# Performance work log

Hardware: AMD Instinct MI355X
Metric: run time of the kernel (lower is better)

The kernel has to match this reference:

```python
import jax, jax.numpy as jnp
import numpy as np

IMG_SIZE = 224
PATCH_SIZE = 16
CONTEXT_LEN = 316
LATENT_DIM = 1024
NUM_HEADS = 16
NUM_PATCHES = (IMG_SIZE // PATCH_SIZE) ** 2  # 196
SEQ_LEN = NUM_PATCHES + CONTEXT_LEN          # 512
BATCH = 8


def prefix_lm_mask(num_img_patches, total):
    # lower-triangular causal mask, but the image-patch block is fully bidirectional
    m = np.tril(np.ones((total, total), dtype=np.float32))
    m[:num_img_patches, :num_img_patches] = 1.0
    return jnp.asarray(m)  # [S, S], 1 = attend, 0 = masked


def setup_inputs() -> dict:
    key = jax.random.key(0)
    k_x, k_q, k_k, k_v, k_o, k_b = jax.random.split(key, 6)
    d = LATENT_DIM
    scale = 1.0 / np.sqrt(d)
    return {
        "x": jax.random.normal(k_x, (BATCH, SEQ_LEN, d), dtype=jnp.float32),
        "w_q": jax.random.normal(k_q, (d, d), dtype=jnp.float32) * scale,
        "w_k": jax.random.normal(k_k, (d, d), dtype=jnp.float32) * scale,
        "w_v": jax.random.normal(k_v, (d, d), dtype=jnp.float32) * scale,
        "w_o": jax.random.normal(k_o, (d, d), dtype=jnp.float32) * scale,
        "b_o": jax.random.normal(k_b, (d,), dtype=jnp.float32) * 0.01,
    }


def reference(x, w_q, w_k, w_v, w_o, b_o):
    B, S, D = x.shape
    H = NUM_HEADS
    hd = D // H
    # projections (nn.Linear: y = x @ W^T)
    q = (x @ w_q.T).reshape(B, S, H, hd).transpose(0, 2, 1, 3)  # [B,H,S,hd]
    k = (x @ w_k.T).reshape(B, S, H, hd).transpose(0, 2, 1, 3)
    v = (x @ w_v.T).reshape(B, S, H, hd).transpose(0, 2, 1, 3)
    scores = jnp.einsum("bhqd,bhkd->bhqk", q, k) / jnp.sqrt(jnp.float32(hd))
    mask = prefix_lm_mask(NUM_PATCHES, S)  # [S,S]
    scores = jnp.where(mask == 0, jnp.float32(-jnp.inf), scores)
    attn = jax.nn.softmax(scores, axis=-1)
    ctx = jnp.einsum("bhqk,bhkd->bhqd", attn, v)
    ctx = ctx.transpose(0, 2, 1, 3).reshape(B, S, D)
    return ctx @ w_o.T + b_o
```

## Files before the change

### kernel.cpp

```cpp
#include <hip/hip_runtime.h>
#include <stdint.h>
#include <math.h>

#define NB_B 8
#define NB_S 512
#define NB_D 1024
#define NB_H 16
#define NB_HD 64
#define NP 196
#define MTOT 4096

#define OFF_XB 0
#define OFF_WQ 4194304
#define OFF_WK 5242880
#define OFF_WV 6291456
#define OFF_WO 7340032
#define OFF_Q  8388608
#define OFF_K  12582912
#define OFF_VT 16777216
#define OFF_CT 20971520

typedef __attribute__((ext_vector_type(8))) short bf16x8;
typedef __attribute__((ext_vector_type(4))) float f32x4;
typedef __attribute__((ext_vector_type(4))) short s16x4;

__device__ __forceinline__ short f2bf(float f) {
  union { float f; uint32_t u; } c; c.f = f;
  uint32_t r = (c.u + 0x7fffu + ((c.u >> 16) & 1u)) >> 16;
  return (short)r;
}

__device__ __forceinline__ uint32_t pack2bf(float lo, float hi) {
  uint32_t ulo = __float_as_uint(lo) + 0x8000u;
  uint32_t uhi = __float_as_uint(hi) + 0x8000u;
  return __builtin_amdgcn_perm(uhi, ulo, 0x07060302u);
}

__device__ __forceinline__ void async16(void* lds, const void* g) {
  __builtin_amdgcn_global_load_lds(
      (const __attribute__((address_space(1))) void*)g,
      (__attribute__((address_space(3))) void*)lds, 16, 0, 0);
}

__global__ __launch_bounds__(256) void cvt5(const float* __restrict__ x,
                                            const float* __restrict__ wq,
                                            const float* __restrict__ wk,
                                            const float* __restrict__ wv,
                                            const float* __restrict__ wo,
                                            short* __restrict__ ws) {
  int b = blockIdx.x, t = threadIdx.x;
  const float* src; short* dst; float scale;
  if (b < 4096) { src = x + b * 1024; dst = ws + OFF_XB + b * 1024; scale = 1.0f; }
  else {
    int wb = b - 4096, wi = wb >> 10, r = wb & 1023;
    switch (wi) {
      case 0:  src = wq + r * 1024; dst = ws + OFF_WQ + r * 1024; scale = 0.125f; break;
      case 1:  src = wk + r * 1024; dst = ws + OFF_WK + r * 1024; scale = 1.0f;   break;
      case 2:  src = wv + r * 1024; dst = ws + OFF_WV + r * 1024; scale = 1.0f;   break;
      default: src = wo + r * 1024; dst = ws + OFF_WO + r * 1024; scale = 1.0f;   break;
    }
  }
  int i = t << 2;
  float4 v = *(const float4*)(src + i);
  s16x4 o;
  o[0] = f2bf(v.x * scale); o[1] = f2bf(v.y * scale);
  o[2] = f2bf(v.z * scale); o[3] = f2bf(v.w * scale);
  *(s16x4*)(dst + i) = o;
}

__global__ __launch_bounds__(256, 2) void gemm_qkv(short* __restrict__ ws) {
  __shared__ __align__(16) short As[4096];
  __shared__ __align__(16) short Bs[4096];
  int bx = blockIdx.x;
  int wsel = bx >> 8;
  int tile = bx & 255;
  int mt = tile >> 3, nt = tile & 7;
  int m0 = mt << 7, n0 = nt << 7;
  const short* A  = ws + OFF_XB;
  const short* Bw = ws + (wsel == 0 ? OFF_WQ : (wsel == 1 ? OFF_WK : OFF_WV));
  int t = threadIdx.x, lane = t & 63, wvi = t >> 6;
  int c = lane & 15, quad = lane >> 4;
  int wm = wvi >> 1, wn = wvi & 1;
  f32x4 acc[4][4] = {};

  for (int kk = 0; kk < 1024; kk += 32) {
#pragma unroll
    for (int i = 0; i < 2; ++i) {
      int ch = wvi * 2 + i;
      const short* ga = A  + (m0 + ch * 16 + c) * 1024 + kk + (quad << 3);
      async16(&As[ch << 9], ga);
      const short* gb = Bw + (n0 + ch * 16 + c) * 1024 + kk + (quad << 3);
      async16(&Bs[ch << 9], gb);
    }
    __syncthreads();
    bf16x8 af[4], bfr[4];
#pragma unroll
    for (int i = 0; i < 4; ++i) af[i]  = *(const bf16x8*)&As[((wm * 4 + i) * 64 + lane) * 8];
#pragma unroll
    for (int j = 0; j < 4; ++j) bfr[j] = *(const bf16x8*)&Bs[((wn * 4 + j) * 64 + lane) * 8];
#pragma unroll
    for (int i = 0; i < 4; ++i)
#pragma unroll
      for (int j = 0; j < 4; ++j)
        acc[i][j] = __builtin_amdgcn_mfma_f32_16x16x32_bf16(af[i], bfr[j], acc[i][j], 0, 0, 0);
    __syncthreads();
  }

  short* outp = ws + (wsel == 0 ? OFF_Q : (wsel == 1 ? OFF_K : OFF_VT));
#pragma unroll
  for (int i = 0; i < 4; ++i) {
#pragma unroll
    for (int j = 0; j < 4; ++j) {
      int n = n0 + wn * 64 + j * 16 + c;
      int h = n >> 6, d = n & 63;
      int mq = m0 + wm * 64 + i * 16 + quad * 4;
      int bb = mq >> 9, s = mq & 511;
      if (wsel < 2) {
#pragma unroll
        for (int r = 0; r < 4; ++r)
          outp[((bb * 16 + h) * 512 + (s + r)) * 64 + d] = f2bf(acc[i][j][r]);
      } else {
        s16x4 o;
#pragma unroll
        for (int r = 0; r < 4; ++r) o[r] = f2bf(acc[i][j][r]);
        *(s16x4*)&outp[((bb * 16 + h) * 64 + d) * 512 + s] = o;
      }
    }
  }
}

__global__ __launch_bounds__(256, 2) void attn(short* __restrict__ ws) {
  __shared__ __align__(16) short Kb[4096];
  __shared__ __align__(16) short Vb[4096];
  int bi = blockIdx.x;
  int bh = bi >> 2, qcr = bi & 3;
  int qc = (qcr + bh + 2 * (bh >> 6)) & 3;
  int t = threadIdx.x, lane = t & 63, wvi = t >> 6;
  int c = lane & 15, quad = lane >> 4;
  const short* Qh  = ws + OFF_Q  + bh * (512 * 64);
  const short* Kh  = ws + OFF_K  + bh * (512 * 64);
  const short* Vth = ws + OFF_VT + bh * (64 * 512);
  short* ctx = ws + OFF_CT;
  int b = bh >> 4, h = bh & 15;

  int qt0 = qc * 128 + wvi * 32;
  int qt1 = qt0 + 16;
  int kn0 = (qt0 + 16 > NP) ? (qt0 + 16) : NP;
  int kn1 = (qt1 + 16 > NP) ? (qt1 + 16) : NP;
  int knb = (qc * 128 + 128 > NP) ? (qc * 128 + 128) : NP;
  int NCH = (knb + 63) >> 6;

  bf16x8 q00 = *(const bf16x8*)(Qh + (qt0 + c) * 64 + (quad << 3));
  bf16x8 q01 = *(const bf16x8*)(Qh + (qt0 + c) * 64 + 32 + (quad << 3));
  bf16x8 q10 = *(const bf16x8*)(Qh + (qt1 + c) * 64 + (quad << 3));
  bf16x8 q11 = *(const bf16x8*)(Qh + (qt1 + c) * 64 + 32 + (quad << 3));

  f32x4 acc0[4] = {}, acc1[4] = {};
  float l0 = 0.0f, l1 = 0.0f;
  int L0 = c + ((quad & 1) << 5);
  bool hilo = quad >= 2;

  for (int ch = 0; ch < NCH; ++ch) {
    int k0 = ch << 6;
    {
      const short* gk = Kh + (k0 + wvi * 16 + c) * 64 + (quad << 3);
      async16(&Kb[(wvi * 2 + 0) << 9], gk);
      async16(&Kb[(wvi * 2 + 1) << 9], gk + 32);
      const short* gv = Vth + (wvi * 16 + c) * 512 + k0 + (quad << 3);
      async16(&Vb[(wvi * 2 + 0) << 9], gv);
      async16(&Vb[(wvi * 2 + 1) << 9], gv + 32);
    }
    __syncthreads();

    bf16x8 ak[4][2], av[4][2];
#pragma unroll
    for (int mb = 0; mb < 4; ++mb)
#pragma unroll
      for (int f = 0; f < 2; ++f) {
        ak[mb][f] = *(const bf16x8*)&Kb[((mb * 2 + f) << 9) + lane * 8];
        av[mb][f] = *(const bf16x8*)&Vb[((mb * 2 + f) << 9) + lane * 8];
      }

#pragma unroll
    for (int s = 0; s < 2; ++s) {
      int qt = s ? qt1 : qt0;
      int kn = s ? kn1 : kn0;
      if (k0 >= kn) continue;
      bf16x8 bq0 = s ? q10 : q00;
      bf16x8 bq1 = s ? q11 : q01;
      f32x4* acc = s ? acc1 : acc0;

      float p[4][4];
#pragma unroll
      for (int mb = 0; mb < 4; ++mb) {
        f32x4 st = {};
        st = __builtin_amdgcn_mfma_f32_16x16x32_bf16(ak[mb][0], bq0, st, 0, 0, 0);
        st = __builtin_amdgcn_mfma_f32_16x16x32_bf16(ak[mb][1], bq1, st, 0, 0, 0);
#pragma unroll
        for (int r = 0; r < 4; ++r) p[mb][r] = __expf(st[r]);
      }

      if ((k0 + 64 > NP) && (k0 + 64 > qt + 1)) {
        int row = qt + c;
#pragma unroll
        for (int mb = 0; mb < 4; ++mb)
#pragma unroll
          for (int r = 0; r < 4; ++r) {
            int key = k0 + mb * 16 + (quad << 2) + r;
            bool v = (row < NP) ? (key < NP) : (key <= row);
            p[mb][r] = v ? p[mb][r] : 0.0f;
          }
      }
      float ls = 0.0f;
#pragma unroll
      for (int mb = 0; mb < 4; ++mb)
#pragma unroll
        for (int r = 0; r < 4; ++r) ls += p[mb][r];
      if (s) l1 += ls; else l0 += ls;

#pragma unroll
      for (int hh = 0; hh < 2; ++hh) {
        float* pa = p[2 * hh];
        float* pb = p[2 * hh + 1];
        uint32_t e0 = pack2bf(pa[0], pa[1]);
        uint32_t e1 = pack2bf(pa[2], pa[3]);
        uint32_t e2 = pack2bf(pb[0], pb[1]);
        uint32_t e3 = pack2bf(pb[2], pb[3]);
        uint32_t a0 = (uint32_t)__shfl((int)e0, L0);
        uint32_t b0 = (uint32_t)__shfl((int)e1, L0);
        uint32_t a1 = (uint32_t)__shfl((int)e0, L0 + 16);
        uint32_t b1 = (uint32_t)__shfl((int)e1, L0 + 16);
        uint32_t c0 = (uint32_t)__shfl((int)e2, L0);
        uint32_t d0 = (uint32_t)__shfl((int)e3, L0);
        uint32_t c1 = (uint32_t)__shfl((int)e2, L0 + 16);
        uint32_t d1 = (uint32_t)__shfl((int)e3, L0 + 16);
        union { uint32_t u[4]; bf16x8 v; } bp;
        bp.u[0] = hilo ? c0 : a0;
        bp.u[1] = hilo ? d0 : b0;
        bp.u[2] = hilo ? c1 : a1;
        bp.u[3] = hilo ? d1 : b1;
#pragma unroll
        for (int db = 0; db < 4; ++db)
          acc[db] = __builtin_amdgcn_mfma_f32_16x16x32_bf16(av[db][hh], bp.v, acc[db], 0, 0, 0);
      }
    }
    __syncthreads();
  }

#pragma unroll
  for (int s = 0; s < 2; ++s) {
    float l = s ? l1 : l0;
    f32x4* acc = s ? acc1 : acc0;
    int qt = s ? qt1 : qt0;
    l += __shfl_xor(l, 16);
    l += __shfl_xor(l, 32);
    float inv = 1.0f / l;
    size_t rowbase = ((size_t)(b * 512 + qt + c)) * 1024 + h * 64 + (quad << 2);
#pragma unroll
    for (int db = 0; db < 4; ++db) {
      s16x4 o;
#pragma unroll
      for (int r = 0; r < 4; ++r) o[r] = f2bf(acc[db][r] * inv);
      *(s16x4*)&ctx[rowbase + db * 16] = o;
    }
  }
}

__global__ __launch_bounds__(256, 2) void gemm_out(const short* __restrict__ ws,
                                                   const float* __restrict__ bias,
                                                   float* __restrict__ out) {
  __shared__ __align__(16) short As[4096];
  __shared__ __align__(16) short Bs[8192];
  int bx = blockIdx.x;
  int mt = bx >> 3, nt = bx & 7;
  int m0 = mt << 6, n0 = nt << 7;
  const short* A  = ws + OFF_CT;
  const short* Bw = ws + OFF_WO;
  int t = threadIdx.x, lane = t & 63, wvi = t >> 6;
  int c = lane & 15, quad = lane >> 4;
  int wm = wvi >> 1, wn = wvi & 1;
  f32x4 acc[2][4] = {};

  for (int kk = 0; kk < 1024; kk += 64) {
#pragma unroll
    for (int i = 0; i < 6; ++i) {
      int ch = wvi * 6 + i;
      if (ch < 8) {
        int mg = ch >> 1, kh = ch & 1;
        async16(&As[ch << 9], A + (m0 + mg * 16 + c) * 1024 + kk + kh * 32 + (quad << 3));
      } else {
        int cb = ch - 8, mg = cb >> 1, kh = cb & 1;
        async16(&Bs[cb << 9], Bw + (n0 + mg * 16 + c) * 1024 + kk + kh * 32 + (quad << 3));
      }
    }
    __syncthreads();

    bf16x8 af[2][2], bfr[4][2];
#pragma unroll
    for (int i = 0; i < 2; ++i)
#pragma unroll
      for (int kh = 0; kh < 2; ++kh)
        af[i][kh] = *(const bf16x8*)&As[((((wm * 2 + i) << 1) + kh) << 9) + lane * 8];
#pragma unroll
    for (int j = 0; j < 4; ++j)
#pragma unroll
      for (int kh = 0; kh < 2; ++kh)
        bfr[j][kh] = *(const bf16x8*)&Bs[((((wn * 4 + j) << 1) + kh) << 9) + lane * 8];
#pragma unroll
    for (int kh = 0; kh < 2; ++kh)
#pragma unroll
      for (int i = 0; i < 2; ++i)
#pragma unroll
        for (int j = 0; j < 4; ++j)
          acc[i][j] = __builtin_amdgcn_mfma_f32_16x16x32_bf16(af[i][kh], bfr[j][kh], acc[i][j], 0, 0, 0);
    __syncthreads();
  }

#pragma unroll
  for (int j = 0; j < 4; ++j) {
    int n = n0 + wn * 64 + j * 16 + c;
    float bj = bias[n];
#pragma unroll
    for (int i = 0; i < 2; ++i) {
      int mq = m0 + wm * 32 + i * 16 + quad * 4;
#pragma unroll
      for (int r = 0; r < 4; ++r)
        out[(size_t)(mq + r) * 1024 + n] = acc[i][j][r] + bj;
    }
  }
}

extern "C" void kernel_launch(void* const* d_in, const int* in_sizes, int n_in,
                              void* d_out, int out_size, void* d_ws, size_t ws_size,
                              hipStream_t stream) {
  (void)in_sizes; (void)n_in; (void)out_size; (void)ws_size;
  const float* x  = (const float*)d_in[0];
  const float* wq = (const float*)d_in[1];
  const float* wk = (const float*)d_in[2];
  const float* wv = (const float*)d_in[3];
  const float* wo = (const float*)d_in[4];
  const float* bo = (const float*)d_in[5];
  short* ws = (short*)d_ws;
  float* out = (float*)d_out;

  cvt5<<<8192, 256, 0, stream>>>(x, wq, wk, wv, wo, ws);
  gemm_qkv<<<768, 256, 0, stream>>>(ws);
  attn<<<512, 256, 0, stream>>>(ws);
  gemm_out<<<512, 256, 0, stream>>>(ws, bo, out);
}
```

Measured before the change: 184.5 us.

## Double-buffer LDS tiles in QKV and output GEMMs with async prefetch

Both GEMM kernels now keep two LDS buffers and issue the async global-to-LDS loads for the next K slice before computing on the current one. Explicit s_waitcnt vmcnt counts and raw s_barrier replace __syncthreads, so only the older batch of loads has to finish before compute starts. This is meant to hide global memory latency behind MFMA work. It doubles LDS use per block, which may reduce occupancy. The hand-written waitcnt counts must match the number of loads each thread issues, or correctness breaks.

```diff
diff --git a/kernel.cpp b/kernel.cpp
--- a/kernel.cpp
+++ b/kernel.cpp
@@ -40,6 +40,10 @@
   __builtin_amdgcn_global_load_lds(
       (const __attribute__((address_space(1))) void*)g,
       (__attribute__((address_space(3))) void*)lds, 16, 0, 0);
+}
+
+__device__ __forceinline__ void barrier_raw() {
+  asm volatile("s_barrier" ::: "memory");
 }
 
 __global__ __launch_bounds__(256) void cvt5(const float* __restrict__ x,
@@ -69,8 +73,8 @@
 }
 
 __global__ __launch_bounds__(256, 2) void gemm_qkv(short* __restrict__ ws) {
-  __shared__ __align__(16) short As[4096];
-  __shared__ __align__(16) short Bs[4096];
+  __shared__ __align__(16) short As[2][4096];
+  __shared__ __align__(16) short Bs[2][4096];
   int bx = blockIdx.x;
   int wsel = bx >> 8;
   int tile = bx & 255;
@@ -83,27 +87,36 @@
   int wm = wvi >> 1, wn = wvi & 1;
   f32x4 acc[4][4] = {};
 
-  for (int kk = 0; kk < 1024; kk += 32) {
+  auto stage = [&](int buf, int kk) {
 #pragma unroll
     for (int i = 0; i < 2; ++i) {
       int ch = wvi * 2 + i;
-      const short* ga = A  + (m0 + ch * 16 + c) * 1024 + kk + (quad << 3);
-      async16(&As[ch << 9], ga);
-      const short* gb = Bw + (n0 + ch * 16 + c) * 1024 + kk + (quad << 3);
-      async16(&Bs[ch << 9], gb);
-    }
-    __syncthreads();
+      async16(&As[buf][ch << 9], A  + (m0 + ch * 16 + c) * 1024 + kk + (quad << 3));
+      async16(&Bs[buf][ch << 9], Bw + (n0 + ch * 16 + c) * 1024 + kk + (quad << 3));
+    }
+  };
+
+  stage(0, 0);
+  for (int it = 0; it < 32; ++it) {
+    int buf = it & 1;
+    if (it < 31) {
+      stage(buf ^ 1, (it + 1) * 32);
+      asm volatile("s_waitcnt vmcnt(4)" ::: "memory");
+    } else {
+      asm volatile("s_waitcnt vmcnt(0)" ::: "memory");
+    }
+    barrier_raw();
     bf16x8 af[4], bfr[4];
 #pragma unroll
-    for (int i = 0; i < 4; ++i) af[i]  = *(const bf16x8*)&As[((wm * 4 + i) * 64 + lane) * 8];
-#pragma unroll
-    for (int j = 0; j < 4; ++j) bfr[j] = *(const bf16x8*)&Bs[((wn * 4 + j) * 64 + lane) * 8];
+    for (int i = 0; i < 4; ++i) af[i]  = *(const bf16x8*)&As[buf][((wm * 4 + i) << 9) + lane * 8];
+#pragma unroll
+    for (int j = 0; j < 4; ++j) bfr[j] = *(const bf16x8*)&Bs[buf][((wn * 4 + j) << 9) + lane * 8];
 #pragma unroll
     for (int i = 0; i < 4; ++i)
 #pragma unroll
       for (int j = 0; j < 4; ++j)
         acc[i][j] = __builtin_amdgcn_mfma_f32_16x16x32_bf16(af[i], bfr[j], acc[i][j], 0, 0, 0);
-    __syncthreads();
+    barrier_raw();
   }
 
   short* outp = ws + (wsel == 0 ? OFF_Q : (wsel == 1 ? OFF_K : OFF_VT));
@@ -269,8 +282,8 @@
 __global__ __launch_bounds__(256, 2) void gemm_out(const short* __restrict__ ws,
                                                    const float* __restrict__ bias,
                                                    float* __restrict__ out) {
-  __shared__ __align__(16) short As[4096];
-  __shared__ __align__(16) short Bs[8192];
+  __shared__ __align__(16) short As[2][4096];
+  __shared__ __align__(16) short Bs[2][8192];
   int bx = blockIdx.x;
   int mt = bx >> 3, nt = bx & 7;
   int m0 = mt << 6, n0 = nt << 7;
@@ -281,31 +294,42 @@
   int wm = wvi >> 1, wn = wvi & 1;
   f32x4 acc[2][4] = {};
 
-  for (int kk = 0; kk < 1024; kk += 64) {
+  auto stage = [&](int buf, int kk) {
 #pragma unroll
     for (int i = 0; i < 6; ++i) {
       int ch = wvi * 6 + i;
       if (ch < 8) {
         int mg = ch >> 1, kh = ch & 1;
-        async16(&As[ch << 9], A + (m0 + mg * 16 + c) * 1024 + kk + kh * 32 + (quad << 3));
+        async16(&As[buf][ch << 9], A + (m0 + mg * 16 + c) * 1024 + kk + kh * 32 + (quad << 3));
       } else {
         int cb = ch - 8, mg = cb >> 1, kh = cb & 1;
-        async16(&Bs[cb << 9], Bw + (n0 + mg * 16 + c) * 1024 + kk + kh * 32 + (quad << 3));
-      }
-    }
-    __syncthreads();
+        async16(&Bs[buf][cb << 9], Bw + (n0 + mg * 16 + c) * 1024 + kk + kh * 32 + (quad << 3));
+      }
+    }
+  };
+
+  stage(0, 0);
+  for (int it = 0; it < 16; ++it) {
+    int buf = it & 1;
+    if (it < 15) {
+      stage(buf ^ 1, (it + 1) * 64);
+      asm volatile("s_waitcnt vmcnt(6)" ::: "memory");
+    } else {
+      asm volatile("s_waitcnt vmcnt(0)" ::: "memory");
+    }
+    barrier_raw();
 
     bf16x8 af[2][2], bfr[4][2];
 #pragma unroll
     for (int i = 0; i < 2; ++i)
 #pragma unroll
       for (int kh = 0; kh < 2; ++kh)
-        af[i][kh] = *(const bf16x8*)&As[((((wm * 2 + i) << 1) + kh) << 9) + lane * 8];
+        af[i][kh] = *(const bf16x8*)&As[buf][((((wm * 2 + i) << 1) + kh) << 9) + lane * 8];
 #pragma unroll
     for (int j = 0; j < 4; ++j)
 #pragma unroll
       for (int kh = 0; kh < 2; ++kh)
-        bfr[j][kh] = *(const bf16x8*)&Bs[((((wn * 4 + j) << 1) + kh) << 9) + lane * 8];
+        bfr[j][kh] = *(const bf16x8*)&Bs[buf][((((wn * 4 + j) << 1) + kh) << 9) + lane * 8];
 #pragma unroll
     for (int kh = 0; kh < 2; ++kh)
 #pragma unroll
@@ -313,7 +337,7 @@
 #pragma unroll
         for (int j = 0; j < 4; ++j)
           acc[i][j] = __builtin_amdgcn_mfma_f32_16x16x32_bf16(af[i][kh], bfr[j][kh], acc[i][j], 0, 0, 0);
-    __syncthreads();
+    barrier_raw();
   }
 
 #pragma unroll
```

New measurement: 182.3 us. About the same (-1.2%).

## Pre-swizzle bf16 operands into MFMA fragment layout for contiguous async loads

Applied to the files above, without the earlier changes.

The conversion kernel now writes x and the four weight matrices into a blocked layout where each 16-row by 32-column tile is stored in exactly the per-lane order the MFMA fragments expect, using 512 larger blocks instead of 8192 small ones. The QKV projection epilogue writes K, V^T and the attention output in matching swizzled layouts, so every async global-to-LDS load in the GEMMs and attention becomes a fully contiguous 1KB wavefront read instead of 16 strided row segments. This is meant to improve global-load coalescing and cut address arithmetic, but the epilogue stores become more scattered, and every producer and consumer of these buffers must agree on the layout.

```diff
diff --git a/kernel.cpp b/kernel.cpp
--- a/kernel.cpp
+++ b/kernel.cpp
@@ -23,6 +23,7 @@
 typedef __attribute__((ext_vector_type(8))) short bf16x8;
 typedef __attribute__((ext_vector_type(4))) float f32x4;
 typedef __attribute__((ext_vector_type(4))) short s16x4;
+typedef __attribute__((ext_vector_type(8))) short s16x8;
 
 __device__ __forceinline__ short f2bf(float f) {
   union { float f; uint32_t u; } c; c.f = f;
@@ -50,22 +51,31 @@
                                             short* __restrict__ ws) {
   int b = blockIdx.x, t = threadIdx.x;
   const float* src; short* dst; float scale;
-  if (b < 4096) { src = x + b * 1024; dst = ws + OFF_XB + b * 1024; scale = 1.0f; }
-  else {
-    int wb = b - 4096, wi = wb >> 10, r = wb & 1023;
-    switch (wi) {
-      case 0:  src = wq + r * 1024; dst = ws + OFF_WQ + r * 1024; scale = 0.125f; break;
-      case 1:  src = wk + r * 1024; dst = ws + OFF_WK + r * 1024; scale = 1.0f;   break;
-      case 2:  src = wv + r * 1024; dst = ws + OFF_WV + r * 1024; scale = 1.0f;   break;
-      default: src = wo + r * 1024; dst = ws + OFF_WO + r * 1024; scale = 1.0f;   break;
-    }
-  }
-  int i = t << 2;
-  float4 v = *(const float4*)(src + i);
-  s16x4 o;
-  o[0] = f2bf(v.x * scale); o[1] = f2bf(v.y * scale);
-  o[2] = f2bf(v.z * scale); o[3] = f2bf(v.w * scale);
-  *(s16x4*)(dst + i) = o;
+  if (b < 256) {
+    src = x + b * 16384;
+    dst = ws + OFF_XB + b * 16384;
+    scale = 1.0f;
+  } else {
+    int wi = (b - 256) >> 6, gn = (b - 256) & 63;
+    const float* wsrc[4] = {wq, wk, wv, wo};
+    src = wsrc[wi] + gn * 16384;
+    dst = ws + OFF_WQ + wi * 1048576 + gn * 16384;
+    scale = (wi == 0) ? 0.125f : 1.0f;
+  }
+#pragma unroll
+  for (int it = 0; it < 8; ++it) {
+    int s = t + it * 256;
+    int kb = s >> 6, l = s & 63, quad = l >> 4, cc = l & 15;
+    const float* sp = src + cc * 1024 + kb * 32 + quad * 8;
+    float4 v0 = *(const float4*)sp;
+    float4 v1 = *(const float4*)(sp + 4);
+    s16x8 o;
+    o[0] = f2bf(v0.x * scale); o[1] = f2bf(v0.y * scale);
+    o[2] = f2bf(v0.z * scale); o[3] = f2bf(v0.w * scale);
+    o[4] = f2bf(v1.x * scale); o[5] = f2bf(v1.y * scale);
+    o[6] = f2bf(v1.z * scale); o[7] = f2bf(v1.w * scale);
+    *(s16x8*)(dst + s * 8) = o;
+  }
 }
 
 __global__ __launch_bounds__(256, 2) void gemm_qkv(short* __restrict__ ws) {
@@ -77,27 +87,27 @@
   int mt = tile >> 3, nt = tile & 7;
   int m0 = mt << 7, n0 = nt << 7;
   const short* A  = ws + OFF_XB;
-  const short* Bw = ws + (wsel == 0 ? OFF_WQ : (wsel == 1 ? OFF_WK : OFF_WV));
+  const short* Bw = ws + OFF_WQ + wsel * 1048576;
   int t = threadIdx.x, lane = t & 63, wvi = t >> 6;
   int c = lane & 15, quad = lane >> 4;
   int wm = wvi >> 1, wn = wvi & 1;
+  int g0 = mt << 3, gn0 = nt << 3;
   f32x4 acc[4][4] = {};
 
   for (int kk = 0; kk < 1024; kk += 32) {
+    int kb = kk >> 5;
 #pragma unroll
     for (int i = 0; i < 2; ++i) {
       int ch = wvi * 2 + i;
-      const short* ga = A  + (m0 + ch * 16 + c) * 1024 + kk + (quad << 3);
-      async16(&As[ch << 9], ga);
-      const short* gb = Bw + (n0 + ch * 16 + c) * 1024 + kk + (quad << 3);
-      async16(&Bs[ch << 9], gb);
+      async16(&As[ch << 9], A  + ((g0  + ch) * 32 + kb) * 512 + lane * 8);
+      async16(&Bs[ch << 9], Bw + ((gn0 + ch) * 32 + kb) * 512 + lane * 8);
     }
     __syncthreads();
     bf16x8 af[4], bfr[4];
 #pragma unroll
-    for (int i = 0; i < 4; ++i) af[i]  = *(const bf16x8*)&As[((wm * 4 + i) * 64 + lane) * 8];
-#pragma unroll
-    for (int j = 0; j < 4; ++j) bfr[j] = *(const bf16x8*)&Bs[((wn * 4 + j) * 64 + lane) * 8];
+    for (int i = 0; i < 4; ++i) af[i]  = *(const bf16x8*)&As[((wm * 4 + i) << 9) + lane * 8];
+#pragma unroll
+    for (int j = 0; j < 4; ++j) bfr[j] = *(const bf16x8*)&Bs[((wn * 4 + j) << 9) + lane * 8];
 #pragma unroll
     for (int i = 0; i < 4; ++i)
 #pragma unroll
@@ -106,7 +116,6 @@
     __syncthreads();
   }
 
-  short* outp = ws + (wsel == 0 ? OFF_Q : (wsel == 1 ? OFF_K : OFF_VT));
 #pragma unroll
   for (int i = 0; i < 4; ++i) {
 #pragma unroll
@@ -114,16 +123,28 @@
       int n = n0 + wn * 64 + j * 16 + c;
       int h = n >> 6, d = n & 63;
       int mq = m0 + wm * 64 + i * 16 + quad * 4;
-      int bb = mq >> 9, s = mq & 511;
-      if (wsel < 2) {
+      int bb = mq >> 9, srow = mq & 511;
+      if (wsel == 0) {
+        short* outp = ws + OFF_Q;
 #pragma unroll
         for (int r = 0; r < 4; ++r)
-          outp[((bb * 16 + h) * 512 + (s + r)) * 64 + d] = f2bf(acc[i][j][r]);
+          outp[((bb * 16 + h) * 512 + srow + r) * 64 + d] = f2bf(acc[i][j][r]);
+      } else if (wsel == 1) {
+        int dblk = d >> 5, qk = (d >> 3) & 3, jd = d & 7;
+        int kg = srow >> 4;
+        size_t base = (size_t)(bb * 16 + h) * 32768 +
+                      (size_t)(((kg * 2 + dblk) * 64 + qk * 16 + quad * 4)) * 8 + jd;
+        short* outp = ws + OFF_K;
+#pragma unroll
+        for (int r = 0; r < 4; ++r) outp[base + r * 8] = f2bf(acc[i][j][r]);
       } else {
+        int dg = d >> 4, cv = d & 15;
+        int kblk = srow >> 5, qv = (srow >> 3) & 3, jv = srow & 7;
         s16x4 o;
 #pragma unroll
         for (int r = 0; r < 4; ++r) o[r] = f2bf(acc[i][j][r]);
-        *(s16x4*)&outp[((bb * 16 + h) * 64 + d) * 512 + s] = o;
+        *(s16x4*)&ws[OFF_VT + (size_t)(bb * 16 + h) * 32768 +
+                     (size_t)((dg * 16 + kblk) * 64 + qv * 16 + cv) * 8 + jv] = o;
       }
     }
   }
@@ -137,10 +158,10 @@
   int qc = (qcr + bh + 2 * (bh >> 6)) & 3;
   int t = threadIdx.x, lane = t & 63, wvi = t >> 6;
   int c = lane & 15, quad = lane >> 4;
-  const short* Qh  = ws + OFF_Q  + bh * (512 * 64);
-  const short* Kh  = ws + OFF_K  + bh * (512 * 64);
-  const short* Vth = ws + OFF_VT + bh * (64 * 512);
-  short* ctx = ws + OFF_CT;
+  const short* Qh   = ws + OFF_Q  + bh * (512 * 64);
+  const short* Ksw  = ws + OFF_K  + (size_t)bh * 32768;
+  const short* Vsw  = ws + OFF_VT + (size_t)bh * 32768;
+  short* ct = ws + OFF_CT;
   int b = bh >> 4, h = bh & 15;
 
   int qt0 = qc * 128 + wvi * 32;
@@ -163,12 +184,14 @@
   for (int ch = 0; ch < NCH; ++ch) {
     int k0 = ch << 6;
     {
-      const short* gk = Kh + (k0 + wvi * 16 + c) * 64 + (quad << 3);
-      async16(&Kb[(wvi * 2 + 0) << 9], gk);
-      async16(&Kb[(wvi * 2 + 1) << 9], gk + 32);
-      const short* gv = Vth + (wvi * 16 + c) * 512 + k0 + (quad << 3);
-      async16(&Vb[(wvi * 2 + 0) << 9], gv);
-      async16(&Vb[(wvi * 2 + 1) << 9], gv + 32);
+      int kg = (k0 >> 4) + wvi;
+#pragma unroll
+      for (int f = 0; f < 2; ++f)
+        async16(&Kb[(wvi * 2 + f) << 9], Ksw + ((kg * 2 + f) * 512) + lane * 8);
+      int kblk = k0 >> 5;
+#pragma unroll
+      for (int f = 0; f < 2; ++f)
+        async16(&Vb[(wvi * 2 + f) << 9], Vsw + ((wvi * 16 + kblk + f) * 512) + lane * 8);
     }
     __syncthreads();
 
@@ -255,13 +278,15 @@
     l += __shfl_xor(l, 16);
     l += __shfl_xor(l, 32);
     float inv = 1.0f / l;
-    size_t rowbase = ((size_t)(b * 512 + qt + c)) * 1024 + h * 64 + (quad << 2);
+    int g = (b * 512 + qt) >> 4;
 #pragma unroll
     for (int db = 0; db < 4; ++db) {
+      int col0 = h * 64 + db * 16 + quad * 4;
+      int kb = col0 >> 5, qp = (col0 & 31) >> 3, jo = col0 & 7;
       s16x4 o;
 #pragma unroll
       for (int r = 0; r < 4; ++r) o[r] = f2bf(acc[db][r] * inv);
-      *(s16x4*)&ctx[rowbase + db * 16] = o;
+      *(s16x4*)&ct[(size_t)((g * 32 + kb) * 64 + qp * 16 + c) * 8 + jo] = o;
     }
   }
 }
@@ -279,18 +304,20 @@
   int t = threadIdx.x, lane = t & 63, wvi = t >> 6;
   int c = lane & 15, quad = lane >> 4;
   int wm = wvi >> 1, wn = wvi & 1;
+  int g0 = m0 >> 4, gn0 = n0 >> 4;
   f32x4 acc[2][4] = {};
 
   for (int kk = 0; kk < 1024; kk += 64) {
+    int kb = kk >> 5;
 #pragma unroll
     for (int i = 0; i < 6; ++i) {
       int ch = wvi * 6 + i;
       if (ch < 8) {
         int mg = ch >> 1, kh = ch & 1;
-        async16(&As[ch << 9], A + (m0 + mg * 16 + c) * 1024 + kk + kh * 32 + (quad << 3));
+        async16(&As[ch << 9], A + ((g0 + mg) * 32 + kb + kh) * 512 + lane * 8);
       } else {
         int cb = ch - 8, mg = cb >> 1, kh = cb & 1;
-        async16(&Bs[cb << 9], Bw + (n0 + mg * 16 + c) * 1024 + kk + kh * 32 + (quad << 3));
+        async16(&Bs[cb << 9], Bw + ((gn0 + mg) * 32 + kb + kh) * 512 + lane * 8);
       }
     }
     __syncthreads();
@@ -343,7 +370,7 @@
   short* ws = (short*)d_ws;
   float* out = (float*)d_out;
 
-  cvt5<<<8192, 256, 0, stream>>>(x, wq, wk, wv, wo, ws);
+  cvt5<<<512, 256, 0, stream>>>(x, wq, wk, wv, wo, ws);
   gemm_qkv<<<768, 256, 0, stream>>>(ws);
   attn<<<512, 256, 0, stream>>>(ws);
   gemm_out<<<512, 256, 0, stream>>>(ws, bo, out);
```

Result: faster. 156.5 us (-15.2%).
